# Optimization experiments

Measured on AMD Instinct MI355X. Metric: run time of the kernel, lower is better.

The kernel has to match this reference:

```python
import jax, jax.numpy as jnp
import numpy as np
import math

N_HEAD = 8
LN_EPS = 1e-5


def _layernorm(x, w, b):
    # Biased variance as in the triton kernel: var = E[x^2] - mean^2
    mean = jnp.mean(x, axis=-1, keepdims=True)
    var = jnp.mean(x * x, axis=-1, keepdims=True) - mean * mean
    return (x - mean) * jax.lax.rsqrt(var + LN_EPS) * w + b


def _gelu_tanh(x):
    # matches triton gelu: tanh approximation
    return 0.5 * x * (1.0 + jnp.tanh(0.7978845608 * (x + 0.044715 * x * x * x)))


def _causal_attention(qkv, n_head):
    B, T, C3 = qkv.shape
    C = C3 // 3
    D = C // n_head
    q, k, v = jnp.split(qkv, 3, axis=-1)
    q = q.reshape(B, T, n_head, D)
    k = k.reshape(B, T, n_head, D)
    v = v.reshape(B, T, n_head, D)
    scale = 1.0 / math.sqrt(D)
    scores = jnp.einsum('bqhd,bkhd->bhqk', q, k) * scale  # [B,H,T,T]
    causal = jnp.tril(jnp.ones((T, T), dtype=bool))
    scores = jnp.where(causal, scores, -jnp.inf)
    p = jax.nn.softmax(scores, axis=-1)
    out = jnp.einsum('bhqk,bkhd->bqhd', p, v)
    return out.reshape(B, T, C)


def setup_inputs() -> dict:
    key = jax.random.key(0)
    ks = jax.random.split(key, 8)
    B, T, C = 8, 2048, 768
    s = 0.02
    return {
        'x': jax.random.normal(ks[0], (B, T, C), jnp.float32),
        'ln1_w': jnp.ones((C,), jnp.float32),
        'ln1_b': jnp.zeros((C,), jnp.float32),
        'w_qkv': jax.random.normal(ks[1], (3 * C, C), jnp.float32) * s,
        'b_qkv': jnp.zeros((3 * C,), jnp.float32),
        'w_attn_proj': jax.random.normal(ks[2], (C, C), jnp.float32) * s,
        'b_attn_proj': jnp.zeros((C,), jnp.float32),
        'ln2_w': jnp.ones((C,), jnp.float32),
        'ln2_b': jnp.zeros((C,), jnp.float32),
        'w_fc': jax.random.normal(ks[3], (4 * C, C), jnp.float32) * s,
        'b_fc': jnp.zeros((4 * C,), jnp.float32),
        'w_mlp_proj': jax.random.normal(ks[4], (C, 4 * C), jnp.float32) * s,
        'b_mlp_proj': jnp.zeros((C,), jnp.float32),
    }


def reference(x, ln1_w, ln1_b, w_qkv, b_qkv, w_attn_proj, b_attn_proj,
              ln2_w, ln2_b, w_fc, b_fc, w_mlp_proj, b_mlp_proj):
    # attention block: fused LN + QKV linear, causal flash attention, out proj, residual
    qkv = _layernorm(x, ln1_w, ln1_b) @ w_qkv.T + b_qkv          # [B,T,3C]
    att = _causal_attention(qkv, N_HEAD)                          # [B,T,C]
    x = x + (att @ w_attn_proj.T + b_attn_proj)
    # MLP block: fused LN + fc + gelu, proj, residual
    h = _gelu_tanh(_layernorm(x, ln2_w, ln2_b) @ w_fc.T + b_fc)   # [B,T,4C]
    x = x + (h @ w_mlp_proj.T + b_mlp_proj)
    return x
```

## Files before the change

### kernel.cpp

```cpp
#include <hip/hip_runtime.h>
#include <hip/hip_bf16.h>
#include <cstdint>
#include <cstddef>

typedef __attribute__((ext_vector_type(8))) short bf16x8;
typedef __attribute__((ext_vector_type(4))) short bf16x4;
typedef __attribute__((ext_vector_type(4))) float f32x4;
typedef __attribute__((ext_vector_type(16))) float f32x16;

#define GLB_AS(p) ((const __attribute__((address_space(1))) void*)(p))
#define LDS_AS(p) ((__attribute__((address_space(3))) void*)(p))

__device__ __forceinline__ short f2bf(float f) {
    union { float f; unsigned u; } x; x.f = f;
    unsigned r = (x.u + 0x7fffu + ((x.u >> 16) & 1u)) >> 16;
    return (short)r;
}
__device__ __forceinline__ unsigned packbf2(float a, float b) {
    union { float f; unsigned u; } x, y; x.f = a; y.f = b;
    return (x.u >> 16) | (y.u & 0xffff0000u);
}
__device__ __forceinline__ f32x4 MF(bf16x8 a, bf16x8 b, f32x4 c) {
    return __builtin_amdgcn_mfma_f32_16x16x32_bf16(a, b, c, 0, 0, 0);
}
__device__ __forceinline__ f32x16 MF32(bf16x8 a, bf16x8 b, f32x16 c) {
    return __builtin_amdgcn_mfma_f32_32x32x16_bf16(a, b, c, 0, 0, 0);
}

__global__ __launch_bounds__(256) void k_cast4(const float* __restrict__ s0,
                                               const float* __restrict__ s1,
                                               const float* __restrict__ s2,
                                               const float* __restrict__ s3,
                                               short* __restrict__ d0,
                                               short* __restrict__ d1,
                                               short* __restrict__ d2,
                                               short* __restrict__ d3,
                                               int n0, int n1, int n2, int n3) {
    const int total = n0 + n1 + n2 + n3;
    int i = blockIdx.x * 256 + threadIdx.x;
    const int stride = gridDim.x * 256;
    for (; i < total; i += stride) {
        int j = i;
        const float* s; short* d;
        if (j < n0) { s = s0; d = d0; }
        else {
            j -= n0;
            if (j < n1) { s = s1; d = d1; }
            else {
                j -= n1;
                if (j < n2) { s = s2; d = d2; }
                else { j -= n2; s = s3; d = d3; }
            }
        }
        float4 v = ((const float4*)s)[j];
        bf16x4 o;
        o[0] = f2bf(v.x); o[1] = f2bf(v.y); o[2] = f2bf(v.z); o[3] = f2bf(v.w);
        ((bf16x4*)d)[j] = o;
    }
}

__global__ __launch_bounds__(256) void k_layernorm(const float* __restrict__ x,
                                                   const float* __restrict__ w,
                                                   const float* __restrict__ b,
                                                   short* __restrict__ out) {
    const int row = blockIdx.x;
    const int tid = threadIdx.x;
    const float* xr = x + (size_t)row * 768;
    float v0 = xr[tid], v1 = xr[tid + 256], v2 = xr[tid + 512];
    float s = v0 + v1 + v2;
    float ss = v0 * v0 + v1 * v1 + v2 * v2;
    #pragma unroll
    for (int m = 32; m; m >>= 1) { s += __shfl_xor(s, m); ss += __shfl_xor(ss, m); }
    __shared__ float red[8];
    int wid = tid >> 6, lane = tid & 63;
    if (lane == 0) { red[wid] = s; red[4 + wid] = ss; }
    __syncthreads();
    s = red[0] + red[1] + red[2] + red[3];
    ss = red[4] + red[5] + red[6] + red[7];
    float mean = s * (1.f / 768.f);
    float var = ss * (1.f / 768.f) - mean * mean;
    float inv = rsqrtf(var + 1e-5f);
    short* orow = out + (size_t)row * 768;
    orow[tid]       = f2bf((v0 - mean) * inv * w[tid]       + b[tid]);
    orow[tid + 256] = f2bf((v1 - mean) * inv * w[tid + 256] + b[tid + 256]);
    orow[tid + 512] = f2bf((v2 - mean) * inv * w[tid + 512] + b[tid + 512]);
}

template <int EPI, int NFR>
__global__ __launch_bounds__(512, 2) void k_gemm256(const short* __restrict__ A,
                                                    const short* __restrict__ B,
                                                    const float* __restrict__ bias,
                                                    const float* __restrict__ res,
                                                    void* __restrict__ out,
                                                    int M, int N, int K) {
    __shared__ short As2[2][256 * 64];
    __shared__ short Bs2[2][NFR * 64 * 64];
    const int tid = threadIdx.x, lane = tid & 63, wid = tid >> 6;
    const int l4 = lane & 15, lh = lane >> 4;
    const int wm = wid >> 2, wn = wid & 3;
    const int gx = gridDim.x;
    const int nwg = gx * gridDim.y;
    int wg = blockIdx.y * gx + blockIdx.x;
    { const int q = nwg >> 3; wg = (wg & 7) * q + (wg >> 3); }
    const int row0 = (wg / gx) * 256, col0 = (wg % gx) * (NFR * 64);

    auto stageA = [&](short* lds, int mh, int k0) {
        #pragma unroll
        for (int i = 0; i < 2; ++i) {
            const int chunk = wid * 2 + i;
            const int dl = mh * 16384 + chunk * 1024 + lane * 16;
            const int r = dl >> 7;
            const int cb = (dl & 127) ^ ((r & 7) << 4);
            __builtin_amdgcn_global_load_lds(
                GLB_AS(A + (size_t)(row0 + r) * K + k0 + (cb >> 1)),
                LDS_AS(lds + mh * 8192 + chunk * 512), 16, 0, 0);
        }
    };
    auto stageB0 = [&](short* lds, int k0) {
        #pragma unroll
        for (int i = 0; i < 2; ++i) {
            const int chunk = wid * 2 + i;
            const int dl = chunk * 1024 + lane * 16;
            const int r = dl >> 7;
            const int cb = (dl & 127) ^ ((r & 7) << 4);
            __builtin_amdgcn_global_load_lds(
                GLB_AS(B + (size_t)(col0 + r) * K + k0 + (cb >> 1)),
                LDS_AS(lds + chunk * 512), 16, 0, 0);
        }
    };
    auto stageB1 = [&](short* lds, int k0) {
        #pragma unroll
        for (int i = 0; i < NFR - 2; ++i) {
            const int chunk = wid * (NFR - 2) + i;
            const int dl = 16384 + chunk * 1024 + lane * 16;
            const int r = dl >> 7;
            const int cb = (dl & 127) ^ ((r & 7) << 4);
            __builtin_amdgcn_global_load_lds(
                GLB_AS(B + (size_t)(col0 + r) * K + k0 + (cb >> 1)),
                LDS_AS(lds + 8192 + chunk * 512), 16, 0, 0);
        }
    };
    auto rd = [&](const short* lds, int r, int kb) -> bf16x8 {
        return *(const bf16x8*)((const char*)lds + r * 128 +
                                ((kb * 64 + lh * 16) ^ ((r & 7) << 4)));
    };

    f32x4 acc[8][NFR] = {};
    bf16x8 a[4][2], b0[2][2], b1[2][2];
    const int NT = K >> 6;

    stageA(As2[0], 0, 0);
    stageA(As2[0], 1, 0);
    stageB0(Bs2[0], 0);
    stageB1(Bs2[0], 0);
    stageB0(Bs2[1], 64);
    stageB1(Bs2[1], 64);
    asm volatile("s_waitcnt vmcnt(%0)" :: "n"(NFR) : "memory");
    __builtin_amdgcn_s_barrier();

    for (int t = 0; t < NT; ++t) {
        const int cur = t & 1, nxt = cur ^ 1;
        const short* Ac = As2[cur];
        const short* Bc = Bs2[cur];
        const int kn = (t + 1) << 6;
        const int kn2 = (t + 2) << 6;
        const bool more1 = (t + 1 < NT);
        const bool more2 = (t + 2 < NT);
        #pragma unroll
        for (int mi = 0; mi < 4; ++mi) {
            const int r = wm * 128 + mi * 16 + l4;
            a[mi][0] = rd(Ac, r, 0); a[mi][1] = rd(Ac, r, 1);
        }
        #pragma unroll
        for (int ni = 0; ni < 2; ++ni) {
            const int r = wn * (NFR * 16) + ni * 16 + l4;
            b0[ni][0] = rd(Bc, r, 0); b0[ni][1] = rd(Bc, r, 1);
        }
        if (more1) stageA(As2[nxt], 0, kn);
        __builtin_amdgcn_s_setprio(1);
        #pragma unroll
        for (int mi = 0; mi < 4; ++mi)
            #pragma unroll
            for (int ni = 0; ni < 2; ++ni) {
                acc[mi][ni] = MF(a[mi][0], b0[ni][0], acc[mi][ni]);
                acc[mi][ni] = MF(a[mi][1], b0[ni][1], acc[mi][ni]);
            }
        __builtin_amdgcn_s_setprio(0);
        __builtin_amdgcn_s_barrier();
        #pragma unroll
        for (int j = 0; j < NFR - 2; ++j) {
            const int r = wn * (NFR * 16) + (2 + j) * 16 + l4;
            b1[j][0] = rd(Bc, r, 0); b1[j][1] = rd(Bc, r, 1);
        }
        if (more1) stageA(As2[nxt], 1, kn);
        __builtin_amdgcn_s_setprio(1);
        #pragma unroll
        for (int mi = 0; mi < 4; ++mi)
            #pragma unroll
            for (int j = 0; j < NFR - 2; ++j) {
                acc[mi][2 + j] = MF(a[mi][0], b1[j][0], acc[mi][2 + j]);
                acc[mi][2 + j] = MF(a[mi][1], b1[j][1], acc[mi][2 + j]);
            }
        __builtin_amdgcn_s_setprio(0);
        __builtin_amdgcn_s_barrier();
        #pragma unroll
        for (int mi = 0; mi < 4; ++mi) {
            const int r = wm * 128 + (4 + mi) * 16 + l4;
            a[mi][0] = rd(Ac, r, 0); a[mi][1] = rd(Ac, r, 1);
        }
        if (more2) stageB0(Bs2[cur], kn2);
        __builtin_amdgcn_s_setprio(1);
        #pragma unroll
        for (int mi = 0; mi < 4; ++mi)
            #pragma unroll
            for (int j = 0; j < NFR - 2; ++j) {
                acc[4 + mi][2 + j] = MF(a[mi][0], b1[j][0], acc[4 + mi][2 + j]);
                acc[4 + mi][2 + j] = MF(a[mi][1], b1[j][1], acc[4 + mi][2 + j]);
            }
        __builtin_amdgcn_s_setprio(0);
        __builtin_amdgcn_s_barrier();
        if (more2) stageB1(Bs2[cur], kn2);
        __builtin_amdgcn_s_setprio(1);
        #pragma unroll
        for (int mi = 0; mi < 4; ++mi)
            #pragma unroll
            for (int ni = 0; ni < 2; ++ni) {
                acc[4 + mi][ni] = MF(a[mi][0], b0[ni][0], acc[4 + mi][ni]);
                acc[4 + mi][ni] = MF(a[mi][1], b0[ni][1], acc[4 + mi][ni]);
            }
        __builtin_amdgcn_s_setprio(0);
        if (more2) {
            asm volatile("s_waitcnt vmcnt(%0)" :: "n"(NFR) : "memory");
        } else if (more1) {
            asm volatile("s_waitcnt vmcnt(0)" ::: "memory");
        }
        __builtin_amdgcn_s_barrier();
    }

    #pragma unroll
    for (int mi = 0; mi < 8; ++mi) {
        const int rowb = row0 + wm * 128 + mi * 16 + lh * 4;
        #pragma unroll
        for (int ni = 0; ni < NFR; ++ni) {
            const int col = col0 + wn * (NFR * 16) + ni * 16 + l4;
            const float bv = bias[col];
            #pragma unroll
            for (int j = 0; j < 4; ++j) {
                const size_t idx = (size_t)(rowb + j) * N + col;
                float v = acc[mi][ni][j] + bv;
                if (EPI == 0) {
                    ((short*)out)[idx] = f2bf(v);
                } else if (EPI == 1) {
                    ((float*)out)[idx] = v + res[idx];
                } else {
                    float u = v + 0.044715f * v * v * v;
                    float t = 1.f - 2.f / (__expf(1.5957691216f * u) + 1.f);
                    ((short*)out)[idx] = f2bf(0.5f * v * (1.f + t));
                }
            }
        }
    }
}

#define ATTN_PROC(QF, O, LROW, QA, Q0)                                         \
    if (kv0 <= (Q0) + 31) {                                                    \
        const bool full = (kv0 + 63 <= (Q0));                                  \
        f32x16 s0 = {}, s1 = {};                                               \
        __builtin_amdgcn_s_setprio(1);                                         \
        _Pragma("unroll")                                                      \
        for (int kb = 0; kb < 6; ++kb) {                                       \
            const int r0 = lq, r1 = 32 + lq;                                   \
            bf16x8 kf0 = *(const bf16x8*)((const char*)&Ks[cur][0] +           \
                          r0 * 256 + ((kb * 32 + hi * 16) ^ ((r0 & 7) << 4))); \
            bf16x8 kf1 = *(const bf16x8*)((const char*)&Ks[cur][0] +           \
                          r1 * 256 + ((kb * 32 + hi * 16) ^ ((r1 & 7) << 4))); \
            s0 = MF32(kf0, QF[kb], s0);                                        \
            s1 = MF32(kf1, QF[kb], s1);                                        \
        }                                                                      \
        __builtin_amdgcn_s_setprio(0);                                         \
        if (!full) {                                                           \
            _Pragma("unroll")                                                  \
            for (int r = 0; r < 16; ++r) {                                     \
                const int kvl = (r & 3) + 8 * (r >> 2) + 4 * hi;               \
                if (kv0 + kvl > (QA)) s0[r] = -INFINITY;                       \
                if (kv0 + 32 + kvl > (QA)) s1[r] = -INFINITY;                  \
            }                                                                  \
        }                                                                      \
        _Pragma("unroll")                                                      \
        for (int r = 0; r < 16; ++r) { s0[r] = exp2f(s0[r]); s1[r] = exp2f(s1[r]); } \
        float ar[16];                                                          \
        _Pragma("unroll")                                                      \
        for (int r = 0; r < 16; ++r) ar[r] = s0[r] + s1[r];                    \
        _Pragma("unroll")                                                      \
        for (int st = 8; st; st >>= 1)                                         \
            _Pragma("unroll")                                                  \
            for (int r = 0; r < 8; ++r)                                        \
                if (r < st) ar[r] += ar[r + st];                               \
        (LROW) += ar[0] + __shfl_xor(ar[0], 32);                               \
        unsigned pk0[8], pk1[8];                                               \
        _Pragma("unroll")                                                      \
        for (int j = 0; j < 8; ++j) {                                          \
            pk0[j] = packbf2(s0[2 * j], s0[2 * j + 1]);                        \
            pk1[j] = packbf2(s1[2 * j], s1[2 * j + 1]);                        \
        }                                                                      \
        __builtin_amdgcn_s_setprio(1);                                         \
        _Pragma("unroll")                                                      \
        for (int db = 0; db < 3; ++db) {                                       \
            const int vrow = db * 32 + lq;                                     \
            const int vsw = ((vrow & 7) ^ ((vrow >> 3) & 7)) << 4;             \
            _Pragma("unroll")                                                  \
            for (int c = 0; c < 4; ++c) {                                      \
                bf16x8 vf = *(const bf16x8*)((const char*)&Vs[cur][0] +        \
                             vrow * 128 + ((c * 32 + hi * 16) ^ vsw));         \
                union { unsigned u[4]; bf16x8 v; } pa;                         \
                const unsigned* pk = (c < 2) ? pk0 : pk1;                      \
                const int o4 = (c & 1) * 4;                                    \
                pa.u[0] = pk[o4]; pa.u[1] = pk[o4 + 1];                        \
                pa.u[2] = pk[o4 + 2]; pa.u[3] = pk[o4 + 3];                    \
                (O)[db] = MF32(vf, pa.v, (O)[db]);                             \
            }                                                                  \
        }                                                                      \
        __builtin_amdgcn_s_setprio(0);                                         \
    }

__global__ __launch_bounds__(256, 2) void k_attn8(const short* __restrict__ qkv,
                                                  short* __restrict__ att) {
    __shared__ short Ks[2][64 * 128];
    __shared__ short Vs[2][96 * 64];
    const int tid = threadIdx.x, lane = tid & 63, wid = tid >> 6;
    const int lq = lane & 31, hi = lane >> 5;
    const int L = blockIdx.x;
    const int h = L & 7, bx = (L >> 3) & 7, b = L >> 6;
    const short* base = qkv + (size_t)b * 2048 * 2304 + h * 96;
    const short* Kb = base + 768;
    const short* Vb = base + 1536;
    const int vkvr = (tid / 12) * 4, vd0 = (tid % 12) * 8;
    const int vslot = (vkvr & ~12) | ((vkvr & 4) << 1) | ((vkvr & 8) >> 1);
    bf16x8 vreg[4];
    const float QSC = 0.14724445f;

    auto stageK = [&](int jt, int bb) {
        const int kv0 = jt * 64;
        for (int c = wid; c < 16; c += 4) {
            const int dl = c * 1024 + lane * 16;
            const int row = dl >> 8;
            const int scol = (dl & 255) ^ ((row & 7) << 4);
            __builtin_amdgcn_global_load_lds(GLB_AS(Kb + (size_t)(kv0 + row) * 2304 + (scol >> 1)),
                                             LDS_AS(&Ks[bb][c * 512]), 16, 0, 0);
        }
    };
    auto loadV = [&](int jt) {
        if (tid < 192) {
            const int kv0 = jt * 64;
            #pragma unroll
            for (int e = 0; e < 4; ++e)
                vreg[e] = *(const bf16x8*)(Vb + (size_t)(kv0 + vkvr + e) * 2304 + vd0);
        }
    };
    auto writeV = [&](int bb) {
        if (tid < 192) {
            #pragma unroll
            for (int f = 0; f < 8; ++f) {
                const int row = vd0 + f;
                const int sw = ((row & 7) ^ ((row >> 3) & 7)) << 4;
                const int byte = (row * 128 + vslot * 2) ^ sw;
                bf16x4 w4;
                w4[0] = vreg[0][f]; w4[1] = vreg[1][f]; w4[2] = vreg[2][f]; w4[3] = vreg[3][f];
                *(bf16x4*)((char*)&Vs[bb][0] + byte) = w4;
            }
        }
    };

    const int qtH = 15 - bx, qtL = bx;
    const int q0H = qtH * 128 + wid * 32, q0L = qtL * 128 + wid * 32;
    const int qaH = q0H + lq, qaL = q0L + lq;

    bf16x8 qfH[6], qfL[6];
    #pragma unroll
    for (int kb = 0; kb < 6; ++kb) {
        bf16x8 vH = *(const bf16x8*)(base + (size_t)qaH * 2304 + kb * 16 + hi * 8);
        bf16x8 vL = *(const bf16x8*)(base + (size_t)qaL * 2304 + kb * 16 + hi * 8);
        #pragma unroll
        for (int e = 0; e < 8; ++e) {
            union { unsigned u; float f; } x, y;
            x.u = ((unsigned)(unsigned short)vH[e]) << 16;
            y.u = ((unsigned)(unsigned short)vL[e]) << 16;
            qfH[kb][e] = f2bf(x.f * QSC);
            qfL[kb][e] = f2bf(y.f * QSC);
        }
    }

    f32x16 oH[3] = {}, oL[3] = {};
    float lrowH = 0.f, lrowL = 0.f;
    const int nt = 2 * qtH + 2;

    stageK(0, 0);
    loadV(0);
    asm volatile("s_waitcnt vmcnt(0)" ::: "memory");
    writeV(0);
    __syncthreads();

    int cur = 0;
    for (int jt = 0; jt < nt; ++jt) {
        const int nxt = cur ^ 1;
        const bool more = (jt + 1 < nt);
        if (more) { stageK(jt + 1, nxt); loadV(jt + 1); }

        const int kv0 = jt * 64;
        ATTN_PROC(qfH, oH, lrowH, qaH, q0H)
        ATTN_PROC(qfL, oL, lrowL, qaL, q0L)

        if (more) {
            asm volatile("s_waitcnt vmcnt(0)" ::: "memory");
            writeV(nxt);
        }
        __syncthreads();
        cur = nxt;
    }

    {
        const float inv = 1.f / lrowH;
        short* orow = att + (size_t)((size_t)b * 2048 + qaH) * 768 + h * 96;
        #pragma unroll
        for (int db = 0; db < 3; ++db)
            #pragma unroll
            for (int j = 0; j < 4; ++j) {
                bf16x4 ov;
                #pragma unroll
                for (int e = 0; e < 4; ++e) ov[e] = f2bf(oH[db][4 * j + e] * inv);
                *(bf16x4*)(orow + db * 32 + 8 * j + 4 * hi) = ov;
            }
    }
    {
        const float inv = 1.f / lrowL;
        short* orow = att + (size_t)((size_t)b * 2048 + qaL) * 768 + h * 96;
        #pragma unroll
        for (int db = 0; db < 3; ++db)
            #pragma unroll
            for (int j = 0; j < 4; ++j) {
                bf16x4 ov;
                #pragma unroll
                for (int e = 0; e < 4; ++e) ov[e] = f2bf(oL[db][4 * j + e] * inv);
                *(bf16x4*)(orow + db * 32 + 8 * j + 4 * hi) = ov;
            }
    }
}

extern "C" void kernel_launch(void* const* d_in, const int* in_sizes, int n_in,
                              void* d_out, int out_size, void* d_ws, size_t ws_size,
                              hipStream_t stream) {
    (void)in_sizes; (void)n_in; (void)out_size; (void)ws_size;
    const float* x      = (const float*)d_in[0];
    const float* ln1_w  = (const float*)d_in[1];
    const float* ln1_b  = (const float*)d_in[2];
    const float* w_qkv  = (const float*)d_in[3];
    const float* b_qkv  = (const float*)d_in[4];
    const float* w_proj = (const float*)d_in[5];
    const float* b_proj = (const float*)d_in[6];
    const float* ln2_w  = (const float*)d_in[7];
    const float* ln2_b  = (const float*)d_in[8];
    const float* w_fc   = (const float*)d_in[9];
    const float* b_fc   = (const float*)d_in[10];
    const float* w_mlp  = (const float*)d_in[11];
    const float* b_mlp  = (const float*)d_in[12];

    const int C = 768, M = 8 * 2048;

    char* ws = (char*)d_ws;
    size_t off = 0;
    auto alloc = [&](size_t bytes) {
        char* p = ws + off;
        off += (bytes + 255) & ~(size_t)255;
        return p;
    };
    short* wqkv_b = (short*)alloc((size_t)3 * C * C * 2);
    short* wproj_b = (short*)alloc((size_t)C * C * 2);
    short* wfc_b  = (short*)alloc((size_t)4 * C * C * 2);
    short* wmlp_b = (short*)alloc((size_t)4 * C * C * 2);
    short* bufA   = (short*)alloc((size_t)M * C * 2);
    short* bufB   = (short*)alloc((size_t)M * 4 * C * 2);
    float* x2     = (float*)alloc((size_t)M * C * 4);

    k_cast4<<<dim3(1728), dim3(256), 0, stream>>>(
        w_qkv, w_proj, w_fc, w_mlp, wqkv_b, wproj_b, wfc_b, wmlp_b,
        3 * C * C / 4, C * C / 4, 4 * C * C / 4, 4 * C * C / 4);

    k_layernorm<<<dim3(M), dim3(256), 0, stream>>>(x, ln1_w, ln1_b, bufA);
    k_gemm256<0, 3><<<dim3(2304 / 192, M / 256), dim3(512), 0, stream>>>(
        bufA, wqkv_b, b_qkv, nullptr, bufB, M, 2304, C);
    k_attn8<<<dim3(512), dim3(256), 0, stream>>>(bufB, bufA);
    k_gemm256<1, 3><<<dim3(768 / 192, M / 256), dim3(512), 0, stream>>>(
        bufA, wproj_b, b_proj, x, x2, M, C, C);
    k_layernorm<<<dim3(M), dim3(256), 0, stream>>>(x2, ln2_w, ln2_b, bufA);
    k_gemm256<2, 4><<<dim3(3072 / 256, M / 256), dim3(512), 0, stream>>>(
        bufA, wfc_b, b_fc, nullptr, bufB, M, 3072, C);
    k_gemm256<1, 3><<<dim3(768 / 192, M / 256), dim3(512), 0, stream>>>(
        bufB, wmlp_b, b_mlp, x2, d_out, M, C, 4 * C);
}
```

Measured before the change: 426.4 us.

## Add 8-phase ping-pong pipelined 256x256 GEMM for the MLP fc layer

Adds a new GEMM kernel that splits each 64-wide K tile into four MFMA quadrant phases. Each phase is separated by barriers and interleaves half-tile global-to-LDS loads with LDS reads, using s_setprio to favour the MFMA blocks. It replaces the previous 256x256 GEMM only for the fc+GELU layer. The goal is finer-grained overlap of memory traffic with matrix math. The cost is many more barriers per iteration and tight hand-managed vmcnt accounting that must stay correct.

```diff
diff --git a/kernel.cpp b/kernel.cpp
--- a/kernel.cpp
+++ b/kernel.cpp
@@ -84,6 +84,192 @@
     orow[tid]       = f2bf((v0 - mean) * inv * w[tid]       + b[tid]);
     orow[tid + 256] = f2bf((v1 - mean) * inv * w[tid + 256] + b[tid + 256]);
     orow[tid + 512] = f2bf((v2 - mean) * inv * w[tid + 512] + b[tid + 512]);
+}
+
+#define QUAD(MB, NB, AA, BB)                                                   \
+    do {                                                                       \
+        __builtin_amdgcn_s_setprio(1);                                         \
+        _Pragma("unroll")                                                      \
+        for (int mi = 0; mi < 4; ++mi)                                         \
+            _Pragma("unroll")                                                  \
+            for (int ni = 0; ni < 2; ++ni) {                                   \
+                acc[(MB) + mi][(NB) + ni] =                                    \
+                    MF(AA[mi][0], BB[ni][0], acc[(MB) + mi][(NB) + ni]);       \
+                acc[(MB) + mi][(NB) + ni] =                                    \
+                    MF(AA[mi][1], BB[ni][1], acc[(MB) + mi][(NB) + ni]);       \
+            }                                                                  \
+        __builtin_amdgcn_s_setprio(0);                                         \
+    } while (0)
+
+#define PH_SYNC()                                                              \
+    __builtin_amdgcn_s_barrier();                                              \
+    asm volatile("s_waitcnt lgkmcnt(0)" ::: "memory");                         \
+    __builtin_amdgcn_sched_barrier(0)
+
+template <int EPI>
+__global__ __launch_bounds__(512, 2) void k_gemm8p(const short* __restrict__ A,
+                                                   const short* __restrict__ B,
+                                                   const float* __restrict__ bias,
+                                                   const float* __restrict__ res,
+                                                   void* __restrict__ out,
+                                                   int M, int N, int K) {
+    __shared__ short As2[2][256 * 64];
+    __shared__ short Bs2[2][256 * 64];
+    const int tid = threadIdx.x, lane = tid & 63, wid = tid >> 6;
+    const int l4 = lane & 15, lh = lane >> 4;
+    const int wm = wid >> 2, wn = wid & 3;
+    const int gx = gridDim.x;
+    const int nwg = gx * gridDim.y;
+    int wg = blockIdx.y * gx + blockIdx.x;
+    { const int q = nwg >> 3; wg = (wg & 7) * q + (wg >> 3); }
+    const int row0 = (wg / gx) * 256, col0 = (wg % gx) * 256;
+
+    auto stage = [&](const short* __restrict__ src, int base_row, short* lds,
+                     int half, int k0) {
+        #pragma unroll
+        for (int i = 0; i < 2; ++i) {
+            const int chunk = wid * 2 + i;
+            const int dl = half * 16384 + chunk * 1024 + lane * 16;
+            const int r = dl >> 7;
+            const int cb = (dl & 127) ^ ((r & 7) << 4);
+            __builtin_amdgcn_global_load_lds(
+                GLB_AS(src + (size_t)(base_row + r) * K + k0 + (cb >> 1)),
+                LDS_AS(lds + half * 8192 + chunk * 512), 16, 0, 0);
+        }
+    };
+    auto rd = [&](const short* lds, int r, int kb) -> bf16x8 {
+        return *(const bf16x8*)((const char*)lds + r * 128 +
+                                ((kb * 64 + lh * 16) ^ ((r & 7) << 4)));
+    };
+
+    f32x4 acc[8][4] = {};
+    bf16x8 a[4][2], b0[2][2], b1[2][2];
+    const int NT = K >> 6;
+
+    stage(B, col0, Bs2[0], 0, 0);
+    stage(A, row0, As2[0], 0, 0);
+    stage(B, col0, Bs2[0], 1, 0);
+    stage(A, row0, As2[0], 1, 0);
+    stage(B, col0, Bs2[1], 0, 64);
+    stage(A, row0, As2[1], 0, 64);
+    asm volatile("s_waitcnt vmcnt(4)" ::: "memory");
+    __builtin_amdgcn_s_barrier();
+
+    for (int it = 0; it < (NT >> 1); ++it) {
+        const int k1 = (2 * it + 1) << 6;
+        const int k2 = (2 * it + 2) << 6;
+        const int k3 = (2 * it + 3) << 6;
+        const bool more = (2 * it + 2 < NT);
+        const short* A0 = As2[0];
+        const short* B0 = Bs2[0];
+        const short* A1 = As2[1];
+        const short* B1 = Bs2[1];
+
+        #pragma unroll
+        for (int mi = 0; mi < 4; ++mi) {
+            const int r = wm * 128 + mi * 16 + l4;
+            a[mi][0] = rd(A0, r, 0); a[mi][1] = rd(A0, r, 1);
+        }
+        #pragma unroll
+        for (int ni = 0; ni < 2; ++ni) {
+            const int r = wn * 64 + ni * 16 + l4;
+            b0[ni][0] = rd(B0, r, 0); b0[ni][1] = rd(B0, r, 1);
+        }
+        stage(B, col0, Bs2[1], 1, k1);
+        PH_SYNC();
+        QUAD(0, 0, a, b0);
+        __builtin_amdgcn_s_barrier();
+        #pragma unroll
+        for (int ni = 0; ni < 2; ++ni) {
+            const int r = wn * 64 + (2 + ni) * 16 + l4;
+            b1[ni][0] = rd(B0, r, 0); b1[ni][1] = rd(B0, r, 1);
+        }
+        stage(A, row0, As2[1], 1, k1);
+        PH_SYNC();
+        QUAD(0, 2, a, b1);
+        __builtin_amdgcn_s_barrier();
+        #pragma unroll
+        for (int mi = 0; mi < 4; ++mi) {
+            const int r = wm * 128 + (4 + mi) * 16 + l4;
+            a[mi][0] = rd(A0, r, 0); a[mi][1] = rd(A0, r, 1);
+        }
+        if (more) stage(B, col0, Bs2[0], 0, k2);
+        PH_SYNC();
+        QUAD(4, 2, a, b1);
+        __builtin_amdgcn_s_barrier();
+        if (more) stage(A, row0, As2[0], 0, k2);
+        PH_SYNC();
+        QUAD(4, 0, a, b0);
+        if (more) {
+            asm volatile("s_waitcnt vmcnt(4)" ::: "memory");
+        } else {
+            asm volatile("s_waitcnt vmcnt(0)" ::: "memory");
+        }
+        __builtin_amdgcn_s_barrier();
+        #pragma unroll
+        for (int mi = 0; mi < 4; ++mi) {
+            const int r = wm * 128 + mi * 16 + l4;
+            a[mi][0] = rd(A1, r, 0); a[mi][1] = rd(A1, r, 1);
+        }
+        #pragma unroll
+        for (int ni = 0; ni < 2; ++ni) {
+            const int r = wn * 64 + ni * 16 + l4;
+            b0[ni][0] = rd(B1, r, 0); b0[ni][1] = rd(B1, r, 1);
+        }
+        if (more) stage(B, col0, Bs2[0], 1, k2);
+        PH_SYNC();
+        QUAD(0, 0, a, b0);
+        __builtin_amdgcn_s_barrier();
+        #pragma unroll
+        for (int ni = 0; ni < 2; ++ni) {
+            const int r = wn * 64 + (2 + ni) * 16 + l4;
+            b1[ni][0] = rd(B1, r, 0); b1[ni][1] = rd(B1, r, 1);
+        }
+        if (more) stage(A, row0, As2[0], 1, k2);
+        PH_SYNC();
+        QUAD(0, 2, a, b1);
+        __builtin_amdgcn_s_barrier();
+        #pragma unroll
+        for (int mi = 0; mi < 4; ++mi) {
+            const int r = wm * 128 + (4 + mi) * 16 + l4;
+            a[mi][0] = rd(A1, r, 0); a[mi][1] = rd(A1, r, 1);
+        }
+        if (more) stage(B, col0, Bs2[1], 0, k3);
+        PH_SYNC();
+        QUAD(4, 2, a, b1);
+        __builtin_amdgcn_s_barrier();
+        if (more) stage(A, row0, As2[1], 0, k3);
+        PH_SYNC();
+        QUAD(4, 0, a, b0);
+        if (more) {
+            asm volatile("s_waitcnt vmcnt(4)" ::: "memory");
+        }
+        __builtin_amdgcn_s_barrier();
+    }
+
+    #pragma unroll
+    for (int mi = 0; mi < 8; ++mi) {
+        const int rowb = row0 + wm * 128 + mi * 16 + lh * 4;
+        #pragma unroll
+        for (int ni = 0; ni < 4; ++ni) {
+            const int col = col0 + wn * 64 + ni * 16 + l4;
+            const float bv = bias[col];
+            #pragma unroll
+            for (int j = 0; j < 4; ++j) {
+                const size_t idx = (size_t)(rowb + j) * N + col;
+                float v = acc[mi][ni][j] + bv;
+                if (EPI == 0) {
+                    ((short*)out)[idx] = f2bf(v);
+                } else if (EPI == 1) {
+                    ((float*)out)[idx] = v + res[idx];
+                } else {
+                    float u = v + 0.044715f * v * v * v;
+                    float t = 1.f - 2.f / (__expf(1.5957691216f * u) + 1.f);
+                    ((short*)out)[idx] = f2bf(0.5f * v * (1.f + t));
+                }
+            }
+        }
+    }
 }
 
 template <int EPI, int NFR>
@@ -492,7 +678,7 @@
     k_gemm256<1, 3><<<dim3(768 / 192, M / 256), dim3(512), 0, stream>>>(
         bufA, wproj_b, b_proj, x, x2, M, C, C);
     k_layernorm<<<dim3(M), dim3(256), 0, stream>>>(x2, ln2_w, ln2_b, bufA);
-    k_gemm256<2, 4><<<dim3(3072 / 256, M / 256), dim3(512), 0, stream>>>(
+    k_gemm8p<2><<<dim3(3072 / 256, M / 256), dim3(512), 0, stream>>>(
         bufA, wfc_b, b_fc, nullptr, bufB, M, 3072, C);
     k_gemm256<1, 3><<<dim3(768 / 192, M / 256), dim3(512), 0, stream>>>(
         bufB, wmlp_b, b_mlp, x2, d_out, M, C, 4 * C);
```

Measured after the change: 432.3 us. About the same (+1.4%).
